# Optimization experiments

Hardware: AMD Instinct MI355X
Metric: run time of the kernel (lower is better)

## Reference

```python
import jax, jax.numpy as jnp
import numpy as np

B, S = 2, 2048
HID = 5120
H = 16
Q_LORA = 1536
KV_LORA = 512
D_ROPE = 64
D_NOPE = 128
D_V = 128
D_Q = D_NOPE + D_ROPE  # 192
SCALE = 1.0 / (D_Q ** 0.5)
EPS = 1e-6
THETA = 10000.0


def rms_norm(x, w):
    var = jnp.mean(jnp.square(x), axis=-1, keepdims=True)
    return x * jax.lax.rsqrt(var + EPS) * w


def rotate_half(x):
    x1, x2 = jnp.split(x, 2, axis=-1)
    return jnp.concatenate((-x2, x1), axis=-1)


def deinterleave(x):
    # view(b,h,s,d//2,2).transpose(4,3).reshape(b,h,s,d)
    b, h, s, d = x.shape
    return x.reshape(b, h, s, d // 2, 2).transpose(0, 1, 2, 4, 3).reshape(b, h, s, d)


def setup_inputs() -> dict:
    key = jax.random.key(0)
    ks = jax.random.split(key, 8)
    hidden_states = jax.random.normal(ks[0], (B, S, HID), dtype=jnp.float32)
    # additive causal mask [B,1,S,S]
    causal = jnp.triu(jnp.full((S, S), -1e9, dtype=jnp.float32), k=1)
    attention_mask = jnp.broadcast_to(causal[None, None], (B, 1, S, S))
    position_ids = jnp.broadcast_to(jnp.arange(S, dtype=jnp.int64), (B, S))
    sd = 0.02
    wq_a = jax.random.normal(ks[1], (Q_LORA, HID), dtype=jnp.float32) * sd
    q_a_ln_w = jnp.ones((Q_LORA,), dtype=jnp.float32)
    wq_b = jax.random.normal(ks[2], (H * D_Q, Q_LORA), dtype=jnp.float32) * sd
    wkv_a = jax.random.normal(ks[3], (KV_LORA + D_ROPE, HID), dtype=jnp.float32) * sd
    kv_a_ln_w = jnp.ones((KV_LORA,), dtype=jnp.float32)
    wkv_b = jax.random.normal(ks[4], (H * (D_NOPE + D_V), KV_LORA), dtype=jnp.float32) * sd
    wo = jax.random.normal(ks[5], (HID, H * D_V), dtype=jnp.float32) * sd
    # rotary tables [S, D_ROPE]
    inv_freq = 1.0 / (THETA ** (jnp.arange(0, D_ROPE, 2, dtype=jnp.float32) / D_ROPE))
    freqs = jnp.arange(S, dtype=jnp.float32)[:, None] * inv_freq[None, :]
    emb = jnp.concatenate((freqs, freqs), axis=-1)
    return {
        'hidden_states': hidden_states,
        'attention_mask': attention_mask,
        'position_ids': position_ids,
        'wq_a': wq_a, 'q_a_ln_w': q_a_ln_w, 'wq_b': wq_b,
        'wkv_a': wkv_a, 'kv_a_ln_w': kv_a_ln_w, 'wkv_b': wkv_b,
        'wo': wo,
        'cos': jnp.cos(emb), 'sin': jnp.sin(emb),
    }


def reference(hidden_states, attention_mask, position_ids, wq_a, q_a_ln_w, wq_b,
              wkv_a, kv_a_ln_w, wkv_b, wo, cos, sin):
    bsz, q_len, _ = hidden_states.shape
    # Q low-rank path: A proj -> RMSNorm -> B proj
    q = rms_norm(hidden_states @ wq_a.T, q_a_ln_w) @ wq_b.T
    q = q.reshape(bsz, q_len, H, D_Q).transpose(0, 2, 1, 3)  # [B,H,S,Dq]
    q_nope, q_pe = q[..., :D_NOPE], q[..., D_NOPE:]
    # KV compressed path (MQA-style shared rope key)
    ckv = hidden_states @ wkv_a.T  # [B,S,KV_LORA+D_ROPE]
    compressed_kv, k_pe = ckv[..., :KV_LORA], ckv[..., KV_LORA:]
    k_pe = k_pe.reshape(bsz, q_len, 1, D_ROPE).transpose(0, 2, 1, 3)  # [B,1,S,Dr]
    kv = rms_norm(compressed_kv, kv_a_ln_w) @ wkv_b.T
    kv = kv.reshape(bsz, q_len, H, D_NOPE + D_V).transpose(0, 2, 1, 3)
    k_nope, value_states = kv[..., :D_NOPE], kv[..., D_NOPE:]
    # decoupled RoPE with de-interleave reorder
    cos_p = cos[position_ids][:, None]  # [B,1,S,Dr]
    sin_p = sin[position_ids][:, None]
    q_pe = deinterleave(q_pe)
    k_pe = deinterleave(k_pe)
    q_pe = q_pe * cos_p + rotate_half(q_pe) * sin_p
    k_pe = k_pe * cos_p + rotate_half(k_pe) * sin_p
    query_states = jnp.concatenate((q_nope, q_pe), axis=-1)  # [B,H,S,Dq]
    key_states = jnp.concatenate(
        (k_nope, jnp.broadcast_to(k_pe, (bsz, H, q_len, D_ROPE))), axis=-1)
    # eager attention
    attn_weights = jnp.einsum('bhqd,bhkd->bhqk', query_states, key_states) * SCALE
    attn_weights = attn_weights + attention_mask
    attn_weights = jax.nn.softmax(attn_weights.astype(jnp.float32), axis=-1).astype(query_states.dtype)
    attn_output = jnp.einsum('bhqk,bhkd->bhqd', attn_weights, value_states)
    attn_output = attn_output.transpose(0, 2, 1, 3).reshape(bsz, q_len, H * D_V)
    return attn_output @ wo.T
```

## Files before the change

kernel.cpp:

```cpp
#include <hip/hip_runtime.h>
#include <hip/hip_bf16.h>


typedef __attribute__((ext_vector_type(8))) __bf16 bf16x8;
typedef __attribute__((ext_vector_type(4))) __bf16 bf16x4;
typedef __attribute__((ext_vector_type(4))) float f32x4;

#define MFMA_BF16(a, b, c) __builtin_amdgcn_mfma_f32_16x16x32_bf16((a), (b), (c), 0, 0, 0)

__device__ __forceinline__ void async_load16(const void* g, void* l) {
  __builtin_amdgcn_global_load_lds(
      (const __attribute__((address_space(1))) void*)g,
      (__attribute__((address_space(3))) void*)l, 16, 0, 0);
}

__global__ void sniff_k(const unsigned int* __restrict__ u, int* __restrict__ flag) {
  int t = threadIdx.x;
  unsigned v = u[t];
  int e = (v >> 7) & 0xFF;
  int s = (e >= 96 && e <= 160) ? 1 : 0;
#pragma unroll
  for (int off = 32; off >= 1; off >>= 1) s += __shfl_xor(s, off);
  __shared__ int cnt[4];
  if ((t & 63) == 0) cnt[t >> 6] = s;
  __syncthreads();
  if (t == 0) flag[0] = (cnt[0] + cnt[1] + cnt[2] + cnt[3] >= 128) ? 1 : 0;
}

__global__ void convert_k(const void* __restrict__ in, __bf16* __restrict__ out,
                          long n, const int* __restrict__ flagp) {
  const int mode = *flagp;
  const long stride = (long)gridDim.x * blockDim.x;
  for (long t = blockIdx.x * (long)blockDim.x + threadIdx.x; t * 4 < n; t += stride) {
    long i = t * 4;
    if (mode) {
      *(uint2*)(out + i) = ((const uint2*)in)[t];
    } else {
      float4 v = ((const float4*)in)[t];
      out[i + 0] = (__bf16)v.x;
      out[i + 1] = (__bf16)v.y;
      out[i + 2] = (__bf16)v.z;
      out[i + 3] = (__bf16)v.w;
    }
  }
}

template <int BN, int OUTMODE>
__global__ __launch_bounds__(256) void gemm_bt(
    const __bf16* __restrict__ A, const __bf16* __restrict__ B,
    void* __restrict__ Cv, const int* __restrict__ flagp,
    int M, int N, int K, int lda, int ldb, int ldc) {
  constexpr int BM = 128, BK = 32;
  constexpr int NT = (BN == 128) ? 4 : 2;
  __shared__ __align__(16) __bf16 As[BM * BK];
  __shared__ __align__(16) __bf16 Bs[BN * BK];
  const int tid = threadIdx.x;
  const int wave = tid >> 6, lane = tid & 63;
  const int m16 = lane & 15, quad = lane >> 4;
  const int m0 = blockIdx.y * BM, n0 = blockIdx.x * BN;
  const int wm = (wave >> 1) * 64;
  const int wn = (wave & 1) * (BN / 2);
  const int ar = lane >> 2;
  const int ak = (lane & 3) * 8;

  f32x4 acc[4][NT];
#pragma unroll
  for (int mt = 0; mt < 4; ++mt)
#pragma unroll
    for (int nt = 0; nt < NT; ++nt) acc[mt][nt] = (f32x4){0.f, 0.f, 0.f, 0.f};

  for (int k0 = 0; k0 < K; k0 += BK) {
#pragma unroll
    for (int c = 0; c < 2; ++c) {
      int q = wave * 2 + c;
      const __bf16* g = A + (size_t)(m0 + q * 16 + ar) * lda + k0 + ak;
      async_load16(g, (void*)(As + q * 512));
    }
    constexpr int BCH = (BN * BK) / 512;
#pragma unroll
    for (int c = 0; c < BCH / 4; ++c) {
      int q = wave * (BCH / 4) + c;
      const __bf16* g = B + (size_t)(n0 + q * 16 + ar) * ldb + k0 + ak;
      async_load16(g, (void*)(Bs + q * 512));
    }
    __syncthreads();
    bf16x8 af[4], bfv[NT];
#pragma unroll
    for (int mt = 0; mt < 4; ++mt)
      af[mt] = *(const bf16x8*)&As[(wm + mt * 16 + m16) * BK + quad * 8];
#pragma unroll
    for (int nt = 0; nt < NT; ++nt)
      bfv[nt] = *(const bf16x8*)&Bs[(wn + nt * 16 + m16) * BK + quad * 8];
#pragma unroll
    for (int mt = 0; mt < 4; ++mt)
#pragma unroll
      for (int nt = 0; nt < NT; ++nt)
        acc[mt][nt] = MFMA_BF16(af[mt], bfv[nt], acc[mt][nt]);
    __syncthreads();
  }
  bool obf16;
  if constexpr (OUTMODE == 2) obf16 = (*flagp != 0);
  else obf16 = (OUTMODE == 1);
#pragma unroll
  for (int mt = 0; mt < 4; ++mt)
#pragma unroll
    for (int nt = 0; nt < NT; ++nt)
#pragma unroll
      for (int rg = 0; rg < 4; ++rg) {
        size_t row = m0 + wm + mt * 16 + quad * 4 + rg;
        size_t col = n0 + wn + nt * 16 + m16;
        float v = acc[mt][nt][rg];
        if (obf16)
          ((__bf16*)Cv)[row * (size_t)ldc + col] = (__bf16)v;
        else
          ((float*)Cv)[row * (size_t)ldc + col] = v;
      }
}

template <int COLS>
__global__ __launch_bounds__(256) void rms_k(const float* __restrict__ in, int ldin,
                                             const __bf16* __restrict__ w,
                                             __bf16* __restrict__ out, int ldout) {
  constexpr int PER = COLS / 256;
  const int row = blockIdx.x, tid = threadIdx.x;
  const float* x = in + (size_t)row * ldin;
  float v[PER];
  float ss = 0.f;
#pragma unroll
  for (int i = 0; i < PER; ++i) {
    v[i] = x[tid + i * 256];
    ss += v[i] * v[i];
  }
#pragma unroll
  for (int off = 32; off >= 1; off >>= 1) ss += __shfl_xor(ss, off);
  __shared__ float red[4];
  if ((tid & 63) == 0) red[tid >> 6] = ss;
  __syncthreads();
  ss = red[0] + red[1] + red[2] + red[3];
  float sc = rsqrtf(ss / (float)COLS + 1e-6f);
#pragma unroll
  for (int i = 0; i < PER; ++i)
    out[(size_t)row * ldout + tid + i * 256] =
        (__bf16)(v[i] * sc * (float)w[tid + i * 256]);
}

__global__ void prep_k(const __bf16* __restrict__ qb,
                       const float* __restrict__ ckv,
                       const __bf16* __restrict__ kvb,
                       const __bf16* __restrict__ cosp,
                       const __bf16* __restrict__ sinp,
                       __bf16* __restrict__ Qg, __bf16* __restrict__ Kg) {
  const int bs = blockIdx.x;
  const int s = bs & 2047, b = bs >> 11;
  const int d = threadIdx.x;
  float c = 0.f, sn = 0.f, kpe = 0.f;
  if (d >= 128) {
    int i = d - 128;
    c = (float)cosp[s * 64 + i];
    sn = (float)sinp[s * 64 + i];
    const float* ck = ckv + (size_t)bs * 576 + 512;
    if (i < 32)
      kpe = ck[2 * i] * c - ck[2 * i + 1] * sn;
    else {
      int j = i - 32;
      kpe = ck[2 * j + 1] * c + ck[2 * j] * sn;
    }
  }
  for (int h = 0; h < 16; ++h) {
    size_t orow = ((size_t)(b * 16 + h) * 2048 + s) * 192 + d;
    const __bf16* qr = qb + (size_t)bs * 3072 + h * 192;
    float qv;
    if (d < 128)
      qv = (float)qr[d];
    else {
      int i = d - 128;
      if (i < 32)
        qv = (float)qr[128 + 2 * i] * c - (float)qr[128 + 2 * i + 1] * sn;
      else {
        int j = i - 32;
        qv = (float)qr[128 + 2 * j + 1] * c + (float)qr[128 + 2 * j] * sn;
      }
    }
    Qg[orow] = (__bf16)qv;
    float kval = (d < 128) ? (float)kvb[(size_t)bs * 4096 + h * 256 + d] : kpe;
    Kg[orow] = (__bf16)kval;
  }
}

#define ATT_SCALE 0.07216878364870323f

__global__ __launch_bounds__(256, 2) void attn_k(const __bf16* __restrict__ Qg,
                                                 const __bf16* __restrict__ Kg,
                                                 const __bf16* __restrict__ kvb,
                                                 __bf16* __restrict__ Og) {
  constexpr int S = 2048;
  __shared__ __align__(16) __bf16 Ks[64 * 200];
  __shared__ __align__(16) __bf16 Vt[128 * 72];
  __shared__ __align__(16) __bf16 Ps[128 * 72];
  const int L = blockIdx.x + (blockIdx.y << 4);
  const int halfg = L >> 8, idx = L & 255;
  const int xt = halfg ? (idx >> 5) : (15 - (idx >> 5));
  const int bh = idx & 31, b = bh >> 4, h = bh & 15;
  const int i0 = xt * 128;
  const int tid = threadIdx.x, wave = tid >> 6, lane = tid & 63;
  const int m16 = lane & 15, quad = lane >> 4;
  const int sb = (tid & 15) * 4, d0 = (tid >> 4) * 8;

  bf16x8 qf[2][6];
  const __bf16* Qb = Qg + ((size_t)bh * S + i0 + wave * 32) * 192;
#pragma unroll
  for (int mt = 0; mt < 2; ++mt)
#pragma unroll
    for (int kc = 0; kc < 6; ++kc)
      qf[mt][kc] = *(const bf16x8*)(Qb + (mt * 16 + m16) * 192 + kc * 32 + quad * 8);

  f32x4 oacc[2][8];
#pragma unroll
  for (int mt = 0; mt < 2; ++mt)
#pragma unroll
    for (int nt = 0; nt < 8; ++nt) oacc[mt][nt] = (f32x4){0.f, 0.f, 0.f, 0.f};
  float mrow[2][4], lrow[2][4];
#pragma unroll
  for (int mt = 0; mt < 2; ++mt)
#pragma unroll
    for (int rg = 0; rg < 4; ++rg) {
      mrow[mt][rg] = -1e30f;
      lrow[mt][rg] = 0.f;
    }

  const __bf16* Kbase = Kg + (size_t)bh * S * 192;
  const __bf16* Vbase = kvb + (size_t)b * S * 4096 + h * 256 + 128 + d0;
  const int ntl = 2 * xt + 2;

  int krow[6], kcol[6];
#pragma unroll
  for (int c = 0; c < 6; ++c) {
    int chunk = tid + c * 256;
    krow[c] = chunk / 24;
    kcol[c] = (chunk % 24) * 8;
  }

  bf16x8 kr[6], vr[4];
#pragma unroll
  for (int c = 0; c < 6; ++c)
    kr[c] = *(const bf16x8*)(Kbase + (size_t)krow[c] * 192 + kcol[c]);
#pragma unroll
  for (int r = 0; r < 4; ++r)
    vr[r] = *(const bf16x8*)(Vbase + (size_t)(sb + r) * 4096);

  for (int t = 0; t < ntl; ++t) {
    const int kt0 = t * 64;
    __syncthreads();
#pragma unroll
    for (int c = 0; c < 6; ++c)
      *(bf16x8*)&Ks[krow[c] * 200 + kcol[c]] = kr[c];
#pragma unroll
    for (int j = 0; j < 8; ++j) {
      bf16x4 wv = {vr[0][j], vr[1][j], vr[2][j], vr[3][j]};
      *(bf16x4*)&Vt[(d0 + j) * 72 + sb] = wv;
    }
    __syncthreads();
    if (t + 1 < ntl) {
      const __bf16* Kb = Kbase + (size_t)(kt0 + 64) * 192;
#pragma unroll
      for (int c = 0; c < 6; ++c)
        kr[c] = *(const bf16x8*)(Kb + (size_t)krow[c] * 192 + kcol[c]);
      const __bf16* Vb = Vbase + (size_t)(kt0 + 64) * 4096;
#pragma unroll
      for (int r = 0; r < 4; ++r)
        vr[r] = *(const bf16x8*)(Vb + (size_t)(sb + r) * 4096);
    }

    f32x4 sacc[2][4];
#pragma unroll
    for (int mt = 0; mt < 2; ++mt)
#pragma unroll
      for (int nt = 0; nt < 4; ++nt) sacc[mt][nt] = (f32x4){0.f, 0.f, 0.f, 0.f};
#pragma unroll
    for (int kc = 0; kc < 6; ++kc) {
      bf16x8 bv[4];
#pragma unroll
      for (int nt = 0; nt < 4; ++nt)
        bv[nt] = *(const bf16x8*)&Ks[(nt * 16 + m16) * 200 + kc * 32 + quad * 8];
#pragma unroll
      for (int nt = 0; nt < 4; ++nt)
#pragma unroll
        for (int mt = 0; mt < 2; ++mt)
          sacc[mt][nt] = MFMA_BF16(qf[mt][kc], bv[nt], sacc[mt][nt]);
    }
#pragma unroll
    for (int mt = 0; mt < 2; ++mt)
#pragma unroll
      for (int nt = 0; nt < 4; ++nt)
#pragma unroll
        for (int rg = 0; rg < 4; ++rg) {
          int qrow = i0 + wave * 32 + mt * 16 + quad * 4 + rg;
          int kcol2 = kt0 + nt * 16 + m16;
          float sv = sacc[mt][nt][rg] * ATT_SCALE;
          sacc[mt][nt][rg] = (kcol2 > qrow) ? -1e30f : sv;
        }
#pragma unroll
    for (int mt = 0; mt < 2; ++mt)
#pragma unroll
      for (int rg = 0; rg < 4; ++rg) {
        float tm = fmaxf(fmaxf(sacc[mt][0][rg], sacc[mt][1][rg]),
                         fmaxf(sacc[mt][2][rg], sacc[mt][3][rg]));
        tm = fmaxf(tm, __shfl_xor(tm, 1));
        tm = fmaxf(tm, __shfl_xor(tm, 2));
        tm = fmaxf(tm, __shfl_xor(tm, 4));
        tm = fmaxf(tm, __shfl_xor(tm, 8));
        float om = mrow[mt][rg];
        float nm = fmaxf(om, tm);
        float alpha = __expf(om - nm);
        mrow[mt][rg] = nm;
        float rs = 0.f;
#pragma unroll
        for (int nt = 0; nt < 4; ++nt) {
          float p = __expf(sacc[mt][nt][rg] - nm);
          sacc[mt][nt][rg] = p;
          rs += p;
        }
        rs += __shfl_xor(rs, 1);
        rs += __shfl_xor(rs, 2);
        rs += __shfl_xor(rs, 4);
        rs += __shfl_xor(rs, 8);
        lrow[mt][rg] = lrow[mt][rg] * alpha + rs;
#pragma unroll
        for (int nt = 0; nt < 8; ++nt) oacc[mt][nt][rg] *= alpha;
      }
#pragma unroll
    for (int mt = 0; mt < 2; ++mt)
#pragma unroll
      for (int nt = 0; nt < 4; ++nt)
#pragma unroll
        for (int rg = 0; rg < 4; ++rg)
          Ps[(wave * 32 + mt * 16 + quad * 4 + rg) * 72 + nt * 16 + m16] =
              (__bf16)sacc[mt][nt][rg];
#pragma unroll
    for (int kc2 = 0; kc2 < 2; ++kc2) {
      bf16x8 af[2];
#pragma unroll
      for (int mt = 0; mt < 2; ++mt)
        af[mt] = *(const bf16x8*)&Ps[(wave * 32 + mt * 16 + m16) * 72 + kc2 * 32 + quad * 8];
#pragma unroll
      for (int nt = 0; nt < 8; ++nt) {
        bf16x8 bv = *(const bf16x8*)&Vt[(nt * 16 + m16) * 72 + kc2 * 32 + quad * 8];
#pragma unroll
        for (int mt = 0; mt < 2; ++mt)
          oacc[mt][nt] = MFMA_BF16(af[mt], bv, oacc[mt][nt]);
      }
    }
  }
#pragma unroll
  for (int mt = 0; mt < 2; ++mt)
#pragma unroll
    for (int nt = 0; nt < 8; ++nt)
#pragma unroll
      for (int rg = 0; rg < 4; ++rg) {
        int sg = i0 + wave * 32 + mt * 16 + quad * 4 + rg;
        int d = nt * 16 + m16;
        float val = oacc[mt][nt][rg] / lrow[mt][rg];
        Og[((size_t)b * S + sg) * 2048 + h * 128 + d] = (__bf16)val;
      }
}

extern "C" void kernel_launch(void* const* d_in, const int* in_sizes, int n_in,
                              void* d_out, int out_size, void* d_ws, size_t ws_size,
                              hipStream_t stream) {
  char* w0 = (char*)d_ws;
  int* flag = (int*)w0;
  char* w = w0 + 256;
  __bf16* hid_bf = (__bf16*)w;   w += (size_t)4096 * 5120 * 2;
  __bf16* wqa_bf = (__bf16*)w;   w += (size_t)1536 * 5120 * 2;
  __bf16* wqb_bf = (__bf16*)w;   w += (size_t)3072 * 1536 * 2;
  __bf16* wkva_bf = (__bf16*)w;  w += (size_t)576 * 5120 * 2;
  __bf16* wkvb_bf = (__bf16*)w;  w += (size_t)4096 * 512 * 2;
  __bf16* wo_bf = (__bf16*)w;    w += (size_t)5120 * 2048 * 2;
  __bf16* cos_bf = (__bf16*)w;   w += (size_t)2048 * 64 * 2;
  __bf16* sin_bf = (__bf16*)w;   w += (size_t)2048 * 64 * 2;
  __bf16* qln_bf = (__bf16*)w;   w += 4096;
  __bf16* kvln_bf = (__bf16*)w;  w += 4096;
  float* qa = (float*)w;         w += (size_t)4096 * 1536 * 4;
  __bf16* qan = (__bf16*)w;      w += (size_t)4096 * 1536 * 2;
  __bf16* qb = (__bf16*)w;       w += (size_t)4096 * 3072 * 2;
  float* ckv = (float*)w;        w += (size_t)4096 * 576 * 4;
  __bf16* ckvn = (__bf16*)w;     w += (size_t)4096 * 512 * 2;
  __bf16* kvb = (__bf16*)w;      w += (size_t)4096 * 4096 * 2;
  __bf16* Qg = hid_bf;
  __bf16* Kg = wqa_bf;
  __bf16* ao = (__bf16*)qa;

  sniff_k<<<1, 256, 0, stream>>>((const unsigned int*)d_in[0], flag);
  convert_k<<<1024, 256, 0, stream>>>(d_in[0], hid_bf, (long)4096 * 5120, flag);
  convert_k<<<1024, 256, 0, stream>>>(d_in[3], wqa_bf, (long)1536 * 5120, flag);
  convert_k<<<1024, 256, 0, stream>>>(d_in[5], wqb_bf, (long)3072 * 1536, flag);
  convert_k<<<1024, 256, 0, stream>>>(d_in[6], wkva_bf, (long)576 * 5120, flag);
  convert_k<<<1024, 256, 0, stream>>>(d_in[8], wkvb_bf, (long)4096 * 512, flag);
  convert_k<<<1024, 256, 0, stream>>>(d_in[9], wo_bf, (long)5120 * 2048, flag);
  convert_k<<<64, 256, 0, stream>>>(d_in[10], cos_bf, (long)2048 * 64, flag);
  convert_k<<<64, 256, 0, stream>>>(d_in[11], sin_bf, (long)2048 * 64, flag);
  convert_k<<<2, 256, 0, stream>>>(d_in[4], qln_bf, 1536, flag);
  convert_k<<<1, 256, 0, stream>>>(d_in[7], kvln_bf, 512, flag);

  gemm_bt<128, 0><<<dim3(12, 32), 256, 0, stream>>>(hid_bf, wqa_bf, qa, flag, 4096, 1536, 5120, 5120, 5120, 1536);
  rms_k<1536><<<4096, 256, 0, stream>>>(qa, 1536, qln_bf, qan, 1536);
  gemm_bt<128, 1><<<dim3(24, 32), 256, 0, stream>>>(qan, wqb_bf, qb, flag, 4096, 3072, 1536, 1536, 1536, 3072);
  gemm_bt<64, 0><<<dim3(9, 32), 256, 0, stream>>>(hid_bf, wkva_bf, ckv, flag, 4096, 576, 5120, 5120, 5120, 576);
  rms_k<512><<<4096, 256, 0, stream>>>(ckv, 576, kvln_bf, ckvn, 512);
  gemm_bt<128, 1><<<dim3(32, 32), 256, 0, stream>>>(ckvn, wkvb_bf, kvb, flag, 4096, 4096, 512, 512, 512, 4096);
  prep_k<<<4096, 192, 0, stream>>>(qb, ckv, kvb, cos_bf, sin_bf, Qg, Kg);
  attn_k<<<dim3(16, 32), 256, 0, stream>>>(Qg, Kg, kvb, ao);
  gemm_bt<128, 2><<<dim3(40, 32), 256, 0, stream>>>(ao, wo_bf, d_out, flag, 4096, 5120, 2048, 2048, 2048, 5120);
}
```

Before: 915.2 us.

## Shrink attention query tile to 64 rows, fold scale into Q, add lazy rescale

```diff
diff --git a/kernel.cpp b/kernel.cpp
--- a/kernel.cpp
+++ b/kernel.cpp
@@ -143,6 +143,8 @@
     out[(size_t)row * ldout + tid + i * 256] =
         (__bf16)(v[i] * sc * (float)w[tid + i * 256]);
 }
+
+#define QK_SCALE (0.07216878364870323f * 1.4426950408889634f)
 
 __global__ void prep_k(const __bf16* __restrict__ qb,
                        const float* __restrict__ ckv,
@@ -181,56 +183,49 @@
         qv = (float)qr[128 + 2 * j + 1] * c + (float)qr[128 + 2 * j] * sn;
       }
     }
-    Qg[orow] = (__bf16)qv;
+    Qg[orow] = (__bf16)(qv * QK_SCALE);
     float kval = (d < 128) ? (float)kvb[(size_t)bs * 4096 + h * 256 + d] : kpe;
     Kg[orow] = (__bf16)kval;
   }
 }
 
-#define ATT_SCALE 0.07216878364870323f
-
-__global__ __launch_bounds__(256, 2) void attn_k(const __bf16* __restrict__ Qg,
+__global__ __launch_bounds__(256, 3) void attn_k(const __bf16* __restrict__ Qg,
                                                  const __bf16* __restrict__ Kg,
                                                  const __bf16* __restrict__ kvb,
                                                  __bf16* __restrict__ Og) {
   constexpr int S = 2048;
   __shared__ __align__(16) __bf16 Ks[64 * 200];
   __shared__ __align__(16) __bf16 Vt[128 * 72];
-  __shared__ __align__(16) __bf16 Ps[128 * 72];
-  const int L = blockIdx.x + (blockIdx.y << 4);
-  const int halfg = L >> 8, idx = L & 255;
-  const int xt = halfg ? (idx >> 5) : (15 - (idx >> 5));
-  const int bh = idx & 31, b = bh >> 4, h = bh & 15;
-  const int i0 = xt * 128;
+  __shared__ __align__(16) __bf16 Ps[64 * 72];
+  const int L = blockIdx.x + (blockIdx.y << 5);
+  const int xcd = L & 7, m = L >> 3;
+  const int xt = 31 - (m >> 2);
+  const int bh = ((m & 3) << 3) | xcd;
+  const int b = bh >> 4, h = bh & 15;
+  const int i0 = xt * 64;
   const int tid = threadIdx.x, wave = tid >> 6, lane = tid & 63;
   const int m16 = lane & 15, quad = lane >> 4;
   const int sb = (tid & 15) * 4, d0 = (tid >> 4) * 8;
 
-  bf16x8 qf[2][6];
-  const __bf16* Qb = Qg + ((size_t)bh * S + i0 + wave * 32) * 192;
-#pragma unroll
-  for (int mt = 0; mt < 2; ++mt)
-#pragma unroll
-    for (int kc = 0; kc < 6; ++kc)
-      qf[mt][kc] = *(const bf16x8*)(Qb + (mt * 16 + m16) * 192 + kc * 32 + quad * 8);
-
-  f32x4 oacc[2][8];
-#pragma unroll
-  for (int mt = 0; mt < 2; ++mt)
-#pragma unroll
-    for (int nt = 0; nt < 8; ++nt) oacc[mt][nt] = (f32x4){0.f, 0.f, 0.f, 0.f};
-  float mrow[2][4], lrow[2][4];
-#pragma unroll
-  for (int mt = 0; mt < 2; ++mt)
-#pragma unroll
-    for (int rg = 0; rg < 4; ++rg) {
-      mrow[mt][rg] = -1e30f;
-      lrow[mt][rg] = 0.f;
-    }
+  bf16x8 qf[6];
+  const __bf16* Qb = Qg + ((size_t)bh * S + i0 + wave * 16) * 192;
+#pragma unroll
+  for (int kc = 0; kc < 6; ++kc)
+    qf[kc] = *(const bf16x8*)(Qb + m16 * 192 + kc * 32 + quad * 8);
+
+  f32x4 oacc[8];
+#pragma unroll
+  for (int nt = 0; nt < 8; ++nt) oacc[nt] = (f32x4){0.f, 0.f, 0.f, 0.f};
+  float mrow[4], lrow[4];
+#pragma unroll
+  for (int rg = 0; rg < 4; ++rg) {
+    mrow[rg] = -1e30f;
+    lrow[rg] = 0.f;
+  }
 
   const __bf16* Kbase = Kg + (size_t)bh * S * 192;
   const __bf16* Vbase = kvb + (size_t)b * S * 4096 + h * 256 + 128 + d0;
-  const int ntl = 2 * xt + 2;
+  const int ntl = xt + 1;
 
   int krow[6], kcol[6];
 #pragma unroll
@@ -271,11 +266,9 @@
         vr[r] = *(const bf16x8*)(Vb + (size_t)(sb + r) * 4096);
     }
 
-    f32x4 sacc[2][4];
-#pragma unroll
-    for (int mt = 0; mt < 2; ++mt)
-#pragma unroll
-      for (int nt = 0; nt < 4; ++nt) sacc[mt][nt] = (f32x4){0.f, 0.f, 0.f, 0.f};
+    f32x4 sacc[4];
+#pragma unroll
+    for (int nt = 0; nt < 4; ++nt) sacc[nt] = (f32x4){0.f, 0.f, 0.f, 0.f};
 #pragma unroll
     for (int kc = 0; kc < 6; ++kc) {
       bf16x8 bv[4];
@@ -284,84 +277,95 @@
         bv[nt] = *(const bf16x8*)&Ks[(nt * 16 + m16) * 200 + kc * 32 + quad * 8];
 #pragma unroll
       for (int nt = 0; nt < 4; ++nt)
-#pragma unroll
-        for (int mt = 0; mt < 2; ++mt)
-          sacc[mt][nt] = MFMA_BF16(qf[mt][kc], bv[nt], sacc[mt][nt]);
-    }
-#pragma unroll
-    for (int mt = 0; mt < 2; ++mt)
+        sacc[nt] = MFMA_BF16(qf[kc], bv[nt], sacc[nt]);
+    }
+    if (t == ntl - 1) {
 #pragma unroll
       for (int nt = 0; nt < 4; ++nt)
 #pragma unroll
         for (int rg = 0; rg < 4; ++rg) {
-          int qrow = i0 + wave * 32 + mt * 16 + quad * 4 + rg;
-          int kcol2 = kt0 + nt * 16 + m16;
-          float sv = sacc[mt][nt][rg] * ATT_SCALE;
-          sacc[mt][nt][rg] = (kcol2 > qrow) ? -1e30f : sv;
+          int qrow = wave * 16 + quad * 4 + rg;
+          int kcl = nt * 16 + m16;
+          if (kcl > qrow) sacc[nt][rg] = -1e30f;
         }
-#pragma unroll
-    for (int mt = 0; mt < 2; ++mt)
+    }
+    float tm[4];
+#pragma unroll
+    for (int rg = 0; rg < 4; ++rg) {
+      float v = fmaxf(fmaxf(sacc[0][rg], sacc[1][rg]),
+                      fmaxf(sacc[2][rg], sacc[3][rg]));
+      v = fmaxf(v, __shfl_xor(v, 1));
+      v = fmaxf(v, __shfl_xor(v, 2));
+      v = fmaxf(v, __shfl_xor(v, 4));
+      v = fmaxf(v, __shfl_xor(v, 8));
+      tm[rg] = v;
+    }
+    bool nomax = true;
+#pragma unroll
+    for (int rg = 0; rg < 4; ++rg) nomax = nomax && (tm[rg] <= mrow[rg] + 8.f);
+    if (__all(nomax)) {
 #pragma unroll
       for (int rg = 0; rg < 4; ++rg) {
-        float tm = fmaxf(fmaxf(sacc[mt][0][rg], sacc[mt][1][rg]),
-                         fmaxf(sacc[mt][2][rg], sacc[mt][3][rg]));
-        tm = fmaxf(tm, __shfl_xor(tm, 1));
-        tm = fmaxf(tm, __shfl_xor(tm, 2));
-        tm = fmaxf(tm, __shfl_xor(tm, 4));
-        tm = fmaxf(tm, __shfl_xor(tm, 8));
-        float om = mrow[mt][rg];
-        float nm = fmaxf(om, tm);
-        float alpha = __expf(om - nm);
-        mrow[mt][rg] = nm;
         float rs = 0.f;
 #pragma unroll
         for (int nt = 0; nt < 4; ++nt) {
-          float p = __expf(sacc[mt][nt][rg] - nm);
-          sacc[mt][nt][rg] = p;
+          float p = exp2f(sacc[nt][rg] - mrow[rg]);
+          sacc[nt][rg] = p;
           rs += p;
         }
         rs += __shfl_xor(rs, 1);
         rs += __shfl_xor(rs, 2);
         rs += __shfl_xor(rs, 4);
         rs += __shfl_xor(rs, 8);
-        lrow[mt][rg] = lrow[mt][rg] * alpha + rs;
-#pragma unroll
-        for (int nt = 0; nt < 8; ++nt) oacc[mt][nt][rg] *= alpha;
+        lrow[rg] += rs;
       }
-#pragma unroll
-    for (int mt = 0; mt < 2; ++mt)
-#pragma unroll
-      for (int nt = 0; nt < 4; ++nt)
-#pragma unroll
-        for (int rg = 0; rg < 4; ++rg)
-          Ps[(wave * 32 + mt * 16 + quad * 4 + rg) * 72 + nt * 16 + m16] =
-              (__bf16)sacc[mt][nt][rg];
+    } else {
+#pragma unroll
+      for (int rg = 0; rg < 4; ++rg) {
+        float nm = fmaxf(mrow[rg], tm[rg]);
+        float alpha = exp2f(mrow[rg] - nm);
+        mrow[rg] = nm;
+        float rs = 0.f;
+#pragma unroll
+        for (int nt = 0; nt < 4; ++nt) {
+          float p = exp2f(sacc[nt][rg] - nm);
+          sacc[nt][rg] = p;
+          rs += p;
+        }
+        rs += __shfl_xor(rs, 1);
+        rs += __shfl_xor(rs, 2);
+        rs += __shfl_xor(rs, 4);
+        rs += __shfl_xor(rs, 8);
+        lrow[rg] = lrow[rg] * alpha + rs;
+#pragma unroll
+        for (int nt = 0; nt < 8; ++nt) oacc[nt][rg] *= alpha;
+      }
+    }
+#pragma unroll
+    for (int nt = 0; nt < 4; ++nt)
+#pragma unroll
+      for (int rg = 0; rg < 4; ++rg)
+        Ps[(wave * 16 + quad * 4 + rg) * 72 + nt * 16 + m16] =
+            (__bf16)sacc[nt][rg];
 #pragma unroll
     for (int kc2 = 0; kc2 < 2; ++kc2) {
-      bf16x8 af[2];
-#pragma unroll
-      for (int mt = 0; mt < 2; ++mt)
-        af[mt] = *(const bf16x8*)&Ps[(wave * 32 + mt * 16 + m16) * 72 + kc2 * 32 + quad * 8];
+      bf16x8 af = *(const bf16x8*)&Ps[(wave * 16 + m16) * 72 + kc2 * 32 + quad * 8];
 #pragma unroll
       for (int nt = 0; nt < 8; ++nt) {
         bf16x8 bv = *(const bf16x8*)&Vt[(nt * 16 + m16) * 72 + kc2 * 32 + quad * 8];
-#pragma unroll
-        for (int mt = 0; mt < 2; ++mt)
-          oacc[mt][nt] = MFMA_BF16(af[mt], bv, oacc[mt][nt]);
+        oacc[nt] = MFMA_BF16(af, bv, oacc[nt]);
       }
     }
   }
 #pragma unroll
-  for (int mt = 0; mt < 2; ++mt)
-#pragma unroll
-    for (int nt = 0; nt < 8; ++nt)
-#pragma unroll
-      for (int rg = 0; rg < 4; ++rg) {
-        int sg = i0 + wave * 32 + mt * 16 + quad * 4 + rg;
-        int d = nt * 16 + m16;
-        float val = oacc[mt][nt][rg] / lrow[mt][rg];
-        Og[((size_t)b * S + sg) * 2048 + h * 128 + d] = (__bf16)val;
-      }
+  for (int nt = 0; nt < 8; ++nt)
+#pragma unroll
+    for (int rg = 0; rg < 4; ++rg) {
+      int sg = i0 + wave * 16 + quad * 4 + rg;
+      int d = nt * 16 + m16;
+      float val = oacc[nt][rg] / lrow[rg];
+      Og[((size_t)b * S + sg) * 2048 + h * 128 + d] = (__bf16)val;
+    }
 }
 
 extern "C" void kernel_launch(void* const* d_in, const int* in_sizes, int n_in,
@@ -409,6 +413,6 @@
   rms_k<512><<<4096, 256, 0, stream>>>(ckv, 576, kvln_bf, ckvn, 512);
   gemm_bt<128, 1><<<dim3(32, 32), 256, 0, stream>>>(ckvn, wkvb_bf, kvb, flag, 4096, 4096, 512, 512, 512, 4096);
   prep_k<<<4096, 192, 0, stream>>>(qb, ckv, kvb, cos_bf, sin_bf, Qg, Kg);
-  attn_k<<<dim3(16, 32), 256, 0, stream>>>(Qg, Kg, kvb, ao);
+  attn_k<<<dim3(32, 32), 256, 0, stream>>>(Qg, Kg, kvb, ao);
   gemm_bt<128, 2><<<dim3(40, 32), 256, 0, stream>>>(ao, wo_bf, d_out, flag, 4096, 5120, 2048, 2048, 2048, 5120);
 }
```

After: 1.087 ms. +18.8%, slower.
